# Optimization experiments

Measured on AMD Instinct MI355X. Metric: run time of the kernel, lower is better.

The kernel has to match this reference:

```python
import jax, jax.numpy as jnp
import numpy as np

B, C, N, HID = 1, 64, 1024, 128


def setup_inputs() -> dict:
    key = jax.random.key(0)
    k1, k2, k3, k4, k5 = jax.random.split(key, 5)
    x = jax.random.normal(k1, (B, C, N), dtype=jnp.float32)
    # Conv2d(2C -> HID, 1): weight [HID, 2C] (1x1 kernel flattened), bias [HID]
    W1 = jax.random.normal(k2, (HID, 2 * C), dtype=jnp.float32) * (1.0 / np.sqrt(2 * C))
    b1 = jax.random.normal(k3, (HID,), dtype=jnp.float32) * 0.01
    # Conv2d(HID -> 1, 1): weight [HID], bias [1]
    W2 = jax.random.normal(k4, (HID,), dtype=jnp.float32) * (1.0 / np.sqrt(HID))
    b2 = jax.random.normal(k5, (1,), dtype=jnp.float32) * 0.01
    return {"x": x, "W1": W1, "b1": b1, "W2": W2, "b2": b2}


def reference(x, W1, b1, W2, b2):
    # Original: m1[b,c,i,j] = x[b,c,j]; m2[b,c,i,j] = x[b,c,i]; block = cat([m1, m2], dim=1)
    # tanh is elementwise, and the 1x1 conv is linear, so we split W1 into the
    # halves acting on m1 (j-indexed) and m2 (i-indexed) and avoid the explicit
    # O(N^2 * 2C) repeat+concat. The nonlinear hidden tensor [B,HID,N,N] is the
    # same math as Conv2d(tanh(block)).
    c = x.shape[1]
    t = jnp.tanh(x)                                   # [B, C, N]
    pj = jnp.einsum('hc,bcn->bhn', W1[:, :c], t)      # contribution of m1 (varies over j)
    pi = jnp.einsum('hc,bcn->bhn', W1[:, c:], t)      # contribution of m2 (varies over i)
    h = jnp.tanh(pi[:, :, :, None] + pj[:, :, None, :] + b1[None, :, None, None])  # [B,HID,N,N]
    e = jnp.einsum('h,bhij->bij', W2, h) + b2[0]      # [B, N, N]
    return e + jnp.swapaxes(e, 1, 2)
```

## Files before the change

kernel.cpp:

```cpp
#include <hip/hip_runtime.h>
#include <math.h>

#define CN    64
#define NN    1024
#define NOFF  496

__device__ __forceinline__ float tanh_fast(float x) {
    float e = __expf(2.0f * x);
    return 1.0f - 2.0f * __builtin_amdgcn_rcpf(e + 1.0f);
}

__global__ __launch_bounds__(256) void prep_kernel(
    const float* __restrict__ x, const float* __restrict__ W1,
    const float* __restrict__ b1, float2* __restrict__ S2h)
{
    __shared__ float t_s[2][64];
    const int tid = threadIdx.x;
    const int n0  = blockIdx.x * 2;

    if (tid < 64) {
        float2 xv = *(const float2*)&x[tid * NN + n0];
        t_s[0][tid] = tanh_fast(xv.x);
        t_s[1][tid] = tanh_fast(xv.y);
    }
    __syncthreads();

    const int h  = tid & 127;
    const int nl = tid >> 7;
    const float4* wrow = (const float4*)(W1 + h * (2 * CN));

    float pj[4] = {0.f, 0.f, 0.f, 0.f};
    float pi[4] = {0.f, 0.f, 0.f, 0.f};
#pragma unroll
    for (int c4 = 0; c4 < 16; ++c4) {
        float4 tv = *(const float4*)&t_s[nl][c4 * 4];
        float4 wl = wrow[c4];
        float4 wh = wrow[16 + c4];
        const int s = c4 & 3;
        pj[s] = fmaf(wl.x, tv.x, fmaf(wl.y, tv.y, fmaf(wl.z, tv.z, fmaf(wl.w, tv.w, pj[s]))));
        pi[s] = fmaf(wh.x, tv.x, fmaf(wh.y, tv.y, fmaf(wh.z, tv.z, fmaf(wh.w, tv.w, pi[s]))));
    }
    float pjs = (pj[0] + pj[1]) + (pj[2] + pj[3]);
    float pis = (pi[0] + pi[1]) + (pi[2] + pi[3]);
    float U = tanh_fast(pis + b1[h]);
    float V = tanh_fast(pjs);
    S2h[(((h >> 1) * NN) + n0 + nl) * 2 + (h & 1)] = make_float2(U, V);
}

__device__ __forceinline__ void cell_term(
    const float4& A, const float4& B,
    float PAe, float QAe, float PAo, float QAo,
    float pBe, float qBe, float pBo, float qBo, float& a)
{
    float d1e = fmaf(A.x, B.y, 1.f);
    float d2e = fmaf(B.x, A.y, 1.f);
    float De  = d1e * d2e;
    float Ne  = fmaf(PAe, qBe, pBe * QAe);
    float d1o = fmaf(A.z, B.w, 1.f);
    float d2o = fmaf(B.z, A.w, 1.f);
    float Do  = d1o * d2o;
    float No  = fmaf(PAo, qBo, pBo * QAo);
    float Num = fmaf(Ne, Do, No * De);
    a = fmaf(Num, __builtin_amdgcn_rcpf(De * Do), a);
}

template<bool DIAG>
__device__ __forceinline__ void run_chunk(
    const float4* __restrict__ Abase, const float4* __restrict__ Bbase,
    const float2* __restrict__ W2p, int hp0, int hp1,
    int la, int lb, float* acc)
{
#pragma unroll 2
    for (int hp = hp0; hp < hp1; ++hp) {
        const float2 w2 = W2p[hp];
        float4 A[4], B[4];
        float PAe[4], QAe[4], PAo[4], QAo[4];
        float pBe[4], qBe[4], pBo[4], qBo[4];
#pragma unroll
        for (int m = 0; m < 4; ++m) {
            A[m]   = Abase[hp * 32 + la + 8 * m];
            PAe[m] = w2.x * (A[m].x + A[m].y);
            QAe[m] = w2.x * fmaf(A[m].x, A[m].y, 1.f);
            PAo[m] = w2.y * (A[m].z + A[m].w);
            QAo[m] = w2.y * fmaf(A[m].z, A[m].w, 1.f);
        }
#pragma unroll
        for (int n = 0; n < 4; ++n) {
            B[n]   = Bbase[hp * 32 + lb + 8 * n];
            pBe[n] = B[n].x + B[n].y;
            qBe[n] = fmaf(B[n].x, B[n].y, 1.f);
            pBo[n] = B[n].z + B[n].w;
            qBo[n] = fmaf(B[n].z, B[n].w, 1.f);
        }
        if (DIAG) {
            int idx = 0;
#pragma unroll
            for (int m = 0; m < 4; ++m)
#pragma unroll
                for (int n = 0; n < 4; ++n)
                    if (n >= m)
                        cell_term(A[m], B[n], PAe[m], QAe[m], PAo[m], QAo[m],
                                  pBe[n], qBe[n], pBo[n], qBo[n], acc[idx++]);
        } else {
#pragma unroll
            for (int m = 0; m < 4; ++m)
#pragma unroll
                for (int n = 0; n < 4; ++n)
                    cell_term(A[m], B[n], PAe[m], QAe[m], PAo[m], QAo[m],
                              pBe[n], qBe[n], pBo[n], qBo[n], acc[m * 4 + n]);
        }
    }
}

__global__ __launch_bounds__(512, 4) void pair_kernel(
    const float4* __restrict__ S2, const float* __restrict__ W2,
    const float* __restrict__ b2, float* __restrict__ out)
{
    const int id  = blockIdx.x;
    const int tid = threadIdx.x;
    const bool dual = (id < 16);

    int i0, j0;
    if (dual) {
        i0 = (2 * id) * 32; j0 = (2 * id + 1) * 32;
    } else {
        int p = id - 16;
        int r = (int)((1.f + sqrtf(8.f * p + 1.f)) * 0.5f);
        while (r * (r - 1) / 2 > p) --r;
        while (r * (r + 1) / 2 <= p) ++r;
        int c = p - r * (r - 1) / 2;
        i0 = c * 32; j0 = r * 32;
    }

    __shared__ float4 sm[4096];
    {
#pragma unroll
        for (int k = 0; k < 4; ++k) {
            int idx = k * 512 + tid;
            int hp = idx >> 5, seg = idx & 31;
            sm[idx]        = S2[hp * NN + i0 + seg];
            sm[2048 + idx] = S2[hp * NN + j0 + seg];
        }
    }
    __syncthreads();

    const int w = tid >> 6, lane = tid & 63;
    const int la = lane & 7, lb = lane >> 3;
    const float4* SiF = sm;
    const float4* SjF = sm + 2048;
    const float2* W2p = (const float2*)W2;

    float acc[16];
#pragma unroll
    for (int q = 0; q < 16; ++q) acc[q] = 0.f;

    if (dual) {
        const float4* base = (w < 4) ? SiF : SjF;
        const int hp0 = (w & 3) * 16;
        run_chunk<true>(base, base, W2p, hp0, hp0 + 16, la, lb, acc);
    } else {
        run_chunk<false>(SiF, SjF, W2p, 8 * w, 8 * w + 8, la, lb, acc);
    }

    __syncthreads();
    float* buf = (float*)sm;
    const float bias2 = 2.0f * b2[0];

    if (!dual) {
#pragma unroll
        for (int q = 0; q < 16; ++q)
            buf[w * 1024 + q * 64 + lane] = acc[q];
        __syncthreads();

        float* T = (float*)sm + 8192;
        for (int c = tid; c < 1024; c += 512) {
            float v = bias2;
#pragma unroll
            for (int wv = 0; wv < 8; ++wv) v += buf[wv * 1024 + c];
            int q = c >> 6, l2 = c & 63;
            int m = q >> 2, n = q & 3;
            T[((l2 & 7) + 8 * m) * 34 + (l2 >> 3) + 8 * n] = v;
        }
        __syncthreads();

        const int tx = tid & 31, ty = tid >> 5;
        out[(i0 + ty)      * NN + j0 + tx] = T[ty * 34 + tx];
        out[(i0 + ty + 16) * NN + j0 + tx] = T[(ty + 16) * 34 + tx];
        out[(j0 + ty)      * NN + i0 + tx] = T[tx * 34 + ty];
        out[(j0 + ty + 16) * NN + i0 + tx] = T[tx * 34 + ty + 16];
    } else {
#pragma unroll
        for (int q = 0; q < 10; ++q)
            buf[w * 640 + q * 64 + lane] = acc[q];
        __syncthreads();

        float* T0 = (float*)sm + 6144;
        float* T1 = (float*)sm + 7296;
        for (int c = tid; c < 1280; c += 512) {
            int s = (c >= 640) ? 1 : 0;
            int cc = c - 640 * s;
            float v = bias2;
#pragma unroll
            for (int wv = 0; wv < 4; ++wv) v += buf[(s * 4 + wv) * 640 + cc];
            int qq = cc >> 6, l2 = cc & 63;
            int m = (qq >= 4) + (qq >= 7) + (qq >= 9);
            int start = (m == 0) ? 0 : (m == 1) ? 4 : (m == 2) ? 7 : 9;
            int n = qq - start + m;
            int il = (l2 & 7) + 8 * m, jl = (l2 >> 3) + 8 * n;
            float* T = s ? T1 : T0;
            T[il * 34 + jl] = v;
            if (m != n) T[jl * 34 + il] = v;
        }
        __syncthreads();

        const int tx = tid & 31, ty = tid >> 5;
#pragma unroll
        for (int s = 0; s < 2; ++s) {
            const float* T = s ? T1 : T0;
            const int b0 = s ? j0 : i0;
            out[(b0 + ty)      * NN + b0 + tx] = T[ty * 34 + tx];
            out[(b0 + ty + 16) * NN + b0 + tx] = T[(ty + 16) * 34 + tx];
        }
    }
}

extern "C" void kernel_launch(void* const* d_in, const int* in_sizes, int n_in,
                              void* d_out, int out_size, void* d_ws, size_t ws_size,
                              hipStream_t stream)
{
    const float* x  = (const float*)d_in[0];
    const float* W1 = (const float*)d_in[1];
    const float* b1 = (const float*)d_in[2];
    const float* W2 = (const float*)d_in[3];
    const float* b2 = (const float*)d_in[4];
    float* out = (float*)d_out;

    float2* S2h = (float2*)d_ws;
    prep_kernel<<<512, 256, 0, stream>>>(x, W1, b1, S2h);
    pair_kernel<<<512, 512, 0, stream>>>((const float4*)d_ws, W2, b2, out);
}
```

Before: 90.12 us.

## Stream S2 operands directly from global with register prefetch instead of LDS staging

The pair kernel no longer stages the i/j column slices of S2 into shared memory behind a block-wide barrier. Each thread now reads its A and B float4 operands straight from global memory (L2/L1 cached) and double-buffers the next h-pair's values in registers while computing the current one. Shared memory shrinks to what the final reduction and transpose need, which removes the upfront load phase and one barrier and may raise occupancy. The cost is more redundant global and cache traffic, since neighbouring lanes re-read the same float4s, and extra register pressure from the prefetch buffers.

Measured after the change: 91.50 us. Within noise of the previous version (+1.5%).

```diff
diff --git a/kernel.cpp b/kernel.cpp
--- a/kernel.cpp
+++ b/kernel.cpp
@@ -3,7 +3,6 @@
 
 #define CN    64
 #define NN    1024
-#define NOFF  496
 
 __device__ __forceinline__ float tanh_fast(float x) {
     float e = __expf(2.0f * x);
@@ -65,32 +64,36 @@
 }
 
 template<bool DIAG>
-__device__ __forceinline__ void run_chunk(
-    const float4* __restrict__ Abase, const float4* __restrict__ Bbase,
-    const float2* __restrict__ W2p, int hp0, int hp1,
-    int la, int lb, float* acc)
-{
-#pragma unroll 2
-    for (int hp = hp0; hp < hp1; ++hp) {
-        const float2 w2 = W2p[hp];
+__device__ __forceinline__ void run_stream(
+    const float4* __restrict__ pA, const float4* __restrict__ pB,
+    const float2* __restrict__ W2p, int hp0, int hpn, float* acc)
+{
+    float4 An[4], Bn[4];
+#pragma unroll
+    for (int m = 0; m < 4; ++m) { An[m] = pA[8 * m]; Bn[m] = pB[8 * m]; }
+
+    for (int it = 0; it < hpn; ++it) {
         float4 A[4], B[4];
+#pragma unroll
+        for (int m = 0; m < 4; ++m) { A[m] = An[m]; B[m] = Bn[m]; }
+        if (it + 1 < hpn) {
+            pA += NN; pB += NN;
+#pragma unroll
+            for (int m = 0; m < 4; ++m) { An[m] = pA[8 * m]; Bn[m] = pB[8 * m]; }
+        }
+        const float2 w2 = W2p[hp0 + it];
         float PAe[4], QAe[4], PAo[4], QAo[4];
         float pBe[4], qBe[4], pBo[4], qBo[4];
 #pragma unroll
         for (int m = 0; m < 4; ++m) {
-            A[m]   = Abase[hp * 32 + la + 8 * m];
             PAe[m] = w2.x * (A[m].x + A[m].y);
             QAe[m] = w2.x * fmaf(A[m].x, A[m].y, 1.f);
             PAo[m] = w2.y * (A[m].z + A[m].w);
             QAo[m] = w2.y * fmaf(A[m].z, A[m].w, 1.f);
-        }
-#pragma unroll
-        for (int n = 0; n < 4; ++n) {
-            B[n]   = Bbase[hp * 32 + lb + 8 * n];
-            pBe[n] = B[n].x + B[n].y;
-            qBe[n] = fmaf(B[n].x, B[n].y, 1.f);
-            pBo[n] = B[n].z + B[n].w;
-            qBo[n] = fmaf(B[n].z, B[n].w, 1.f);
+            pBe[m] = B[m].x + B[m].y;
+            qBe[m] = fmaf(B[m].x, B[m].y, 1.f);
+            pBo[m] = B[m].z + B[m].w;
+            qBo[m] = fmaf(B[m].z, B[m].w, 1.f);
         }
         if (DIAG) {
             int idx = 0;
@@ -132,22 +135,9 @@
         i0 = c * 32; j0 = r * 32;
     }
 
-    __shared__ float4 sm[4096];
-    {
-#pragma unroll
-        for (int k = 0; k < 4; ++k) {
-            int idx = k * 512 + tid;
-            int hp = idx >> 5, seg = idx & 31;
-            sm[idx]        = S2[hp * NN + i0 + seg];
-            sm[2048 + idx] = S2[hp * NN + j0 + seg];
-        }
-    }
-    __syncthreads();
-
+    __shared__ float smem[9280];
     const int w = tid >> 6, lane = tid & 63;
     const int la = lane & 7, lb = lane >> 3;
-    const float4* SiF = sm;
-    const float4* SjF = sm + 2048;
     const float2* W2p = (const float2*)W2;
 
     float acc[16];
@@ -155,15 +145,19 @@
     for (int q = 0; q < 16; ++q) acc[q] = 0.f;
 
     if (dual) {
-        const float4* base = (w < 4) ? SiF : SjF;
+        const int col = (w < 4) ? i0 : j0;
         const int hp0 = (w & 3) * 16;
-        run_chunk<true>(base, base, W2p, hp0, hp0 + 16, la, lb, acc);
+        run_stream<true>(S2 + (size_t)hp0 * NN + col + la,
+                         S2 + (size_t)hp0 * NN + col + lb,
+                         W2p, hp0, 16, acc);
     } else {
-        run_chunk<false>(SiF, SjF, W2p, 8 * w, 8 * w + 8, la, lb, acc);
-    }
-
-    __syncthreads();
-    float* buf = (float*)sm;
+        const int hp0 = 8 * w;
+        run_stream<false>(S2 + (size_t)hp0 * NN + i0 + la,
+                          S2 + (size_t)hp0 * NN + j0 + lb,
+                          W2p, hp0, 8, acc);
+    }
+
+    float* buf = smem;
     const float bias2 = 2.0f * b2[0];
 
     if (!dual) {
@@ -172,7 +166,7 @@
             buf[w * 1024 + q * 64 + lane] = acc[q];
         __syncthreads();
 
-        float* T = (float*)sm + 8192;
+        float* T = smem + 8192;
         for (int c = tid; c < 1024; c += 512) {
             float v = bias2;
 #pragma unroll
@@ -194,8 +188,8 @@
             buf[w * 640 + q * 64 + lane] = acc[q];
         __syncthreads();
 
-        float* T0 = (float*)sm + 6144;
-        float* T1 = (float*)sm + 7296;
+        float* T0 = smem + 6144;
+        float* T1 = smem + 7296;
         for (int c = tid; c < 1280; c += 512) {
             int s = (c >= 640) ? 1 : 0;
             int cc = c - 640 * s;
```
